# Optimization experiments

Hardware: AMD Instinct MI355X
Metric: run time of the kernel (lower is better)

The kernel has to match this reference:

```python
import jax, jax.numpy as jnp
import numpy as np

B, N, E, D, M, T, P, HS, HN, C, NH = 64, 1024, 512, 1024, 16, 12, 2048, 2048, 64, 4, 8
EPS = 1e-8


def _ln(x, g, b):
    m = x.mean(-1, keepdims=True)
    v = ((x - m) ** 2).mean(-1, keepdims=True)
    return (x - m) / jnp.sqrt(v + 1e-5) * g + b


def _glu(x):
    a, b = jnp.split(x, 2, axis=-1)
    return a * jax.nn.sigmoid(b)


def setup_inputs() -> dict:
    key = jax.random.key(0)
    ks = jax.random.split(key, 24)
    s = 0.02
    rn = lambda k, sh: jax.random.normal(k, sh, jnp.float32) * s
    inp = {
        'kv_tokens': jax.random.normal(ks[0], (B, N, E), jnp.float32),
        'raw_r_act': jnp.full((P,), -10.0, jnp.float32),  # no_decay_init
        'raw_r_out': jnp.full((P,), -10.0, jnp.float32),
        'q_w': rn(ks[1], (E, P)), 'q_b': jnp.zeros((E,), jnp.float32),
        'in_proj_w': rn(ks[2], (3 * E, E)), 'in_proj_b': jnp.zeros((3 * E,), jnp.float32),
        'out_proj_w': rn(ks[3], (E, E)), 'out_proj_b': jnp.zeros((E,), jnp.float32),
        'z_ln_g': jnp.ones((D,), jnp.float32), 'z_ln_b': jnp.zeros((D,), jnp.float32),
        'o_ln_g': jnp.ones((E,), jnp.float32), 'o_ln_b': jnp.zeros((E,), jnp.float32),
        'gate_w': rn(ks[4], (D, D + E)), 'gate_b': jnp.zeros((D,), jnp.float32),
        'cand_w': rn(ks[5], (D, D + E)), 'cand_b': jnp.zeros((D,), jnp.float32),
        'syn1_w': rn(ks[6], (HS, D + E)), 'syn1_b': jnp.zeros((HS,), jnp.float32),
        'syn2_w': rn(ks[7], (D, HS)), 'syn2_b': jnp.zeros((D,), jnp.float32),
        'nlm1_w': rn(ks[8], (D, M, 2 * HN)), 'nlm1_b': jnp.zeros((D, 2 * HN), jnp.float32),
        'nlm2_w': rn(ks[9], (D, HN, 2)), 'nlm2_b': jnp.zeros((D, 2), jnp.float32),
        'head_w': rn(ks[10], (C, P)), 'head_b': jnp.zeros((C,), jnp.float32),
        'act_left': jax.random.randint(ks[11], (P,), 0, D),
        'act_right': jax.random.randint(ks[12], (P,), 0, D),
        'out_left': jax.random.randint(ks[13], (P,), 0, D),
        'out_right': jax.random.randint(ks[14], (P,), 0, D),
    }
    return inp


def reference(kv_tokens, raw_r_act, raw_r_out, q_w, q_b, in_proj_w, in_proj_b,
              out_proj_w, out_proj_b, z_ln_g, z_ln_b, o_ln_g, o_ln_b,
              gate_w, gate_b, cand_w, cand_b, syn1_w, syn1_b, syn2_w, syn2_b,
              nlm1_w, nlm1_b, nlm2_w, nlm2_b, head_w, head_b,
              act_left, act_right, out_left, out_right):
    dh = E // NH
    scale = 1.0 / np.sqrt(dh).astype(np.float32)
    Wq, Wk, Wv = jnp.split(in_proj_w, 3, axis=0)
    bq, bk, bv = jnp.split(in_proj_b, 3, axis=0)
    # K/V are tick-invariant: project once.
    k = (kv_tokens @ Wk.T + bk).reshape(B, N, NH, dh).transpose(0, 2, 1, 3)  # [B,H,N,dh]
    v = (kv_tokens @ Wv.T + bv).reshape(B, N, NH, dh).transpose(0, 2, 1, 3)
    decay_a = jnp.exp(-jax.nn.softplus(raw_r_act))[None, :]
    decay_o = jnp.exp(-jax.nn.softplus(raw_r_out))[None, :]

    z0 = jnp.zeros((B, D), kv_tokens.dtype)
    A0 = jnp.zeros((B, D, M), kv_tokens.dtype)
    # init_state with z0 == 0 -> alpha 0, beta 1, synch 0
    a_a0 = z0[:, act_left] * z0[:, act_right]
    b_a0 = jnp.ones_like(a_a0)
    s_a0 = a_a0 / jnp.sqrt(b_a0 + EPS)
    a_o0 = z0[:, out_left] * z0[:, out_right]
    b_o0 = jnp.ones_like(a_o0)

    def tick(carry, _):
        z, A, a_a, b_a, s_a, a_o, b_o = carry
        # attention query from action sync
        q = s_a @ q_w.T + q_b                                  # [B,E]
        qh = (q @ Wq.T + bq).reshape(B, NH, 1, dh)
        scores = jnp.einsum('bhqd,bhnd->bhqn', qh, k) * scale  # [B,H,1,N]
        attn = jax.nn.softmax(scores, axis=-1)
        o = jnp.einsum('bhqn,bhnd->bhqd', attn, v).reshape(B, E)
        o = o @ out_proj_w.T + out_proj_b
        o = _ln(o, o_ln_g, o_ln_b)                             # LN on o
        zn = _ln(z, z_ln_g, z_ln_b)                            # LN on z
        # gated fusion
        u = jnp.concatenate([zn, o], axis=-1)
        g = jax.nn.sigmoid(u @ gate_w.T + gate_b)
        h = jnp.tanh(u @ cand_w.T + cand_b)
        z_bar = (1.0 - g) * zn + g * h
        fused = jnp.concatenate([z_bar, o], axis=-1)           # [B,D+E]
        # synapse MLP -> pre-activation
        pre = jax.nn.gelu(fused @ syn1_w.T + syn1_b, approximate=False) @ syn2_w.T + syn2_b
        A = jnp.concatenate([A[:, :, 1:], pre[:, :, None]], axis=-1)  # shift history
        # deep NLM (per-neuron SuperLinear + GLU, twice)
        h1 = _glu(jnp.einsum('bdm,dmh->bdh', A, nlm1_w) + nlm1_b)
        z = _glu(jnp.einsum('bdh,dho->bdo', h1, nlm2_w) + nlm2_b)[..., 0]
        # decayed pair synchronisation updates
        a_a = decay_a * a_a + z[:, act_left] * z[:, act_right]
        b_a = decay_a * b_a + 1.0
        s_a = a_a / jnp.sqrt(b_a + EPS)
        a_o = decay_o * a_o + z[:, out_left] * z[:, out_right]
        b_o = decay_o * b_o + 1.0
        s_o = a_o / jnp.sqrt(b_o + EPS)
        logits = s_o @ head_w.T + head_b                       # [B,C]
        return (z, A, a_a, b_a, s_a, a_o, b_o), (logits, z)

    carry0 = (z0, A0, a_a0, b_a0, s_a0, a_o0, b_o0)
    _, (logits_t, z_t) = jax.lax.scan(tick, carry0, None, length=T)
    logits_ticks = jnp.transpose(logits_t, (1, 2, 0))          # [B,C,T]
    p = jnp.clip(jax.nn.softmax(logits_ticks, axis=1), 1e-8, None)
    ent = -(p * jnp.log(p)).sum(axis=1)
    certainty = 1.0 - ent / np.float32(np.log(C))              # [B,T]
    z_ticks = jnp.transpose(z_t, (1, 0, 2))                    # [B,T,D]
    return logits_ticks, certainty, z_ticks
```

## Files before the change

kernel.cpp:

```cpp
#include <hip/hip_runtime.h>
#include <hip/hip_bf16.h>

#define B_ 64
#define N_ 1024
#define E_ 512
#define D_ 1024
#define M_ 16
#define T_ 12
#define P_ 2048
#define HS_ 2048
#define HN_ 64
#define C_ 4
#define NH_ 8
#define DH_ 64

typedef __attribute__((ext_vector_type(8))) short bf16x8;
typedef __attribute__((ext_vector_type(4))) float f32x4;

__device__ __forceinline__ float bf2f(unsigned int u) {
    union { unsigned int i; float f; } c; c.i = (u & 0xffffu) << 16; return c.f;
}
__device__ __forceinline__ unsigned short f2bf(float f) {
    union { float f; unsigned int i; } c; c.f = f;
    unsigned int x = c.i;
    unsigned int r = x + 0x7fffu + ((x >> 16) & 1u);
    return (unsigned short)(r >> 16);
}

__global__ void init_kernel(unsigned short* s_a_bf, float* a_a, float* b_a, float* a_o, float* b_o, float* z) {
    int i = blockIdx.x * 256 + threadIdx.x;
    if (i < B_ * P_) { a_a[i] = 0.f; b_a[i] = 1.f; a_o[i] = 0.f; b_o[i] = 1.f; s_a_bf[i] = 0; }
    if (i < B_ * D_) z[i] = 0.f;
}

__global__ __launch_bounds__(256) void cvt_bf16_kernel(const float* __restrict__ in,
                                                       unsigned short* __restrict__ out, int n4) {
    int i = blockIdx.x * 256 + threadIdx.x;
    if (i < n4) {
        float4 v = ((const float4*)in)[i];
        ushort4 o;
        o.x = f2bf(v.x); o.y = f2bf(v.y); o.z = f2bf(v.z); o.w = f2bf(v.w);
        ((ushort4*)out)[i] = o;
    }
}

__global__ __launch_bounds__(256) void cvt_ilv_kernel(const float* __restrict__ g,
                                                      const float* __restrict__ c,
                                                      unsigned short* __restrict__ out) {
    int r = blockIdx.x;
    const float* src = (r & 1) ? (c + (size_t)(r >> 1) * 1536) : (g + (size_t)(r >> 1) * 1536);
    for (int k = threadIdx.x * 4; k < 1536; k += 1024) {
        float4 v = *(const float4*)(src + k);
        ushort4 o;
        o.x = f2bf(v.x); o.y = f2bf(v.y); o.z = f2bf(v.z); o.w = f2bf(v.w);
        *(ushort4*)(out + (size_t)r * 1536 + k) = o;
    }
}

__global__ __launch_bounds__(256) void transpose_cvt_kernel(const float* __restrict__ in,
                                                            unsigned short* __restrict__ out,
                                                            int R, int Ccols) {
    __shared__ float tb[32][33];
    int c0 = blockIdx.x * 32, r0 = blockIdx.y * 32;
    int tx = threadIdx.x & 31, ty = threadIdx.x >> 5;
#pragma unroll
    for (int i = 0; i < 32; i += 8) tb[ty + i][tx] = in[(size_t)(r0 + ty + i) * Ccols + c0 + tx];
    __syncthreads();
#pragma unroll
    for (int i = 0; i < 32; i += 8) out[(size_t)(c0 + ty + i) * R + r0 + tx] = f2bf(tb[tx][ty + i]);
}

__global__ __launch_bounds__(256) void bcomb_kernel(const float* __restrict__ in_proj_w,
                                                    const float* __restrict__ in_proj_b,
                                                    const float* __restrict__ q_b,
                                                    float* __restrict__ bc) {
    int e = blockIdx.x * 256 + threadIdx.x;
    if (e < E_) {
        const float* wr = in_proj_w + (size_t)e * E_;
        float s = in_proj_b[e];
        for (int k = 0; k < E_; k += 4) {
            float4 w4 = *(const float4*)(wr + k);
            float4 q4 = *(const float4*)(q_b + k);
            s += w4.x * q4.x + w4.y * q4.y + w4.z * q4.z + w4.w * q4.w;
        }
        bc[e] = s;
    }
}

template <bool HAS_BIAS>
__global__ __launch_bounds__(256) void gemm_bt_kernel(const unsigned short* __restrict__ A,
                                                      const unsigned short* __restrict__ Bt,
                                                      const float* __restrict__ bias,
                                                      unsigned short* __restrict__ C,
                                                      int M, int N, int K) {
    __shared__ __align__(16) unsigned short ldsA[2][4096];
    __shared__ __align__(16) unsigned short ldsB[2][4096];
    int id = blockIdx.y * gridDim.x + blockIdx.x;
    int nwg = gridDim.x * gridDim.y;
    int swz = (id & 7) * (nwg >> 3) + (id >> 3);
    int bx = swz % gridDim.x, by = swz / gridDim.x;
    int m0 = by * 128;
    int n0 = bx * 128;
    int tid = threadIdx.x;
    int wv = tid >> 6, l = tid & 63;
    int wr = wv >> 1, wc = wv & 1;
    int lr = l & 15, lg = l >> 4;
    f32x4 acc[4][4] = {};

    auto stage = [&](int buf, int kt) {
        int k0 = kt * 32;
#pragma unroll
        for (int i = 0; i < 2; i++) {
            int tsk = tid + 256 * i;
            int r = tsk >> 2, g = tsk & 3;
            int gs = (g ^ (r & 3)) * 8;
            __builtin_amdgcn_global_load_lds(
                (const __attribute__((address_space(1))) void*)(A + (size_t)(m0 + r) * K + k0 + gs),
                (__attribute__((address_space(3))) void*)&ldsA[buf][tsk * 8], 16, 0, 0);
        }
#pragma unroll
        for (int i = 0; i < 2; i++) {
            int tsk = tid + 256 * i;
            int r = tsk >> 2, g = tsk & 3;
            int gs = (g ^ (r & 3)) * 8;
            __builtin_amdgcn_global_load_lds(
                (const __attribute__((address_space(1))) void*)(Bt + (size_t)(n0 + r) * K + k0 + gs),
                (__attribute__((address_space(3))) void*)&ldsB[buf][tsk * 8], 16, 0, 0);
        }
    };

    int nt = K >> 5;
    stage(0, 0);
    for (int t = 0; t < nt; t++) {
        int cur = t & 1;
        if (t + 1 < nt) {
            stage(cur ^ 1, t + 1);
            asm volatile("s_waitcnt vmcnt(4)" ::: "memory");
        } else {
            asm volatile("s_waitcnt vmcnt(0)" ::: "memory");
        }
        __builtin_amdgcn_s_barrier();
        bf16x8 af[4], bfr[4];
#pragma unroll
        for (int mi = 0; mi < 4; mi++) {
            int r = wr * 64 + mi * 16 + lr;
            af[mi] = *(const bf16x8*)&ldsA[cur][r * 32 + ((lg ^ (r & 3)) << 3)];
        }
#pragma unroll
        for (int ni = 0; ni < 4; ni++) {
            int c = wc * 64 + ni * 16 + lr;
            bfr[ni] = *(const bf16x8*)&ldsB[cur][c * 32 + ((lg ^ (c & 3)) << 3)];
        }
#pragma unroll
        for (int mi = 0; mi < 4; mi++)
#pragma unroll
            for (int ni = 0; ni < 4; ni++)
                acc[mi][ni] = __builtin_amdgcn_mfma_f32_16x16x32_bf16(af[mi], bfr[ni], acc[mi][ni], 0, 0, 0);
        __builtin_amdgcn_s_barrier();
    }
#pragma unroll
    for (int ni = 0; ni < 4; ni++) {
        int col = n0 + wc * 64 + ni * 16 + lr;
        float bv = HAS_BIAS ? bias[col] : 0.0f;
#pragma unroll
        for (int mi = 0; mi < 4; mi++) {
            int row = m0 + wr * 64 + mi * 16 + lg * 4;
#pragma unroll
            for (int r = 0; r < 4; r++) {
                C[(size_t)(row + r) * N + col] = f2bf(acc[mi][ni][r] + bv);
            }
        }
    }
}

template <int EPI>
__global__ __launch_bounds__(256) void gemmNK_kernel(const unsigned short* __restrict__ A,
                                                     const unsigned short* __restrict__ W,
                                                     const float* __restrict__ bias0,
                                                     const float* __restrict__ bias1,
                                                     const float* __restrict__ zn32,
                                                     void* __restrict__ outp,
                                                     int N, int K) {
    __shared__ __align__(16) unsigned short ldsA[4][2][2048];
    __shared__ __align__(16) unsigned short ldsB[4][2][512];
    int n0 = blockIdx.x * 16;
    int tid = threadIdx.x;
    int w = tid >> 6, l = tid & 63;
    int Kw = K >> 2;
    int kb = w * Kw;
    int lr = l & 15, lg = l >> 4;
    int ar = l >> 2, ag = l & 3;
    f32x4 acc[4] = {};

    auto stage = [&](int buf, int kt) {
        int k0 = kb + (kt << 5);
#pragma unroll
        for (int i = 0; i < 4; i++) {
            int row = i * 16 + ar;
            int gs = (ag ^ (row & 3)) << 3;
            __builtin_amdgcn_global_load_lds(
                (const __attribute__((address_space(1))) void*)(A + (size_t)row * K + k0 + gs),
                (__attribute__((address_space(3))) void*)&ldsA[w][buf][i * 512 + l * 8], 16, 0, 0);
        }
        {
            int col = ar;
            int gs = (ag ^ (col & 3)) << 3;
            __builtin_amdgcn_global_load_lds(
                (const __attribute__((address_space(1))) void*)(W + (size_t)(n0 + col) * K + k0 + gs),
                (__attribute__((address_space(3))) void*)&ldsB[w][buf][l * 8], 16, 0, 0);
        }
    };

    int nt = Kw >> 5;
    stage(0, 0);
    for (int t = 0; t < nt; t++) {
        int cur = t & 1;
        if (t + 1 < nt) {
            stage(cur ^ 1, t + 1);
            asm volatile("s_waitcnt vmcnt(5)" ::: "memory");
        } else {
            asm volatile("s_waitcnt vmcnt(0)" ::: "memory");
        }
        bf16x8 bf = *(const bf16x8*)&ldsB[w][cur][lr * 32 + ((lg ^ (lr & 3)) << 3)];
#pragma unroll
        for (int mi = 0; mi < 4; mi++) {
            int rr = mi * 16 + lr;
            bf16x8 af = *(const bf16x8*)&ldsA[w][cur][rr * 32 + ((lg ^ (rr & 3)) << 3)];
            acc[mi] = __builtin_amdgcn_mfma_f32_16x16x32_bf16(af, bf, acc[mi], 0, 0, 0);
        }
    }
    __syncthreads();
    float* red = (float*)&ldsA[0][0][0];
#pragma unroll
    for (int mi = 0; mi < 4; mi++) {
        int row = mi * 16 + lg * 4;
#pragma unroll
        for (int q = 0; q < 4; q++) red[w * 1024 + (row + q) * 16 + lr] = acc[mi][q];
    }
    __syncthreads();
    int b = tid >> 2, c4 = (tid & 3) << 2;
    f32x4 s = *(f32x4*)&red[b * 16 + c4];
#pragma unroll
    for (int ww = 1; ww < 4; ww++) {
        f32x4 v = *(f32x4*)&red[ww * 1024 + b * 16 + c4];
        s[0] += v[0]; s[1] += v[1]; s[2] += v[2]; s[3] += v[3];
    }
    int col = n0 + c4;
    if (EPI == 0) {
        unsigned short* out = (unsigned short*)outp;
        ushort4 o;
        o.x = f2bf(s[0] + bias0[col + 0]);
        o.y = f2bf(s[1] + bias0[col + 1]);
        o.z = f2bf(s[2] + bias0[col + 2]);
        o.w = f2bf(s[3] + bias0[col + 3]);
        *(ushort4*)(out + (size_t)b * N + col) = o;
    } else if (EPI == 1) {
        float* out = (float*)outp;
        *(f32x4*)(out + (size_t)b * N + col) = s;
    } else if (EPI == 2) {
        unsigned short* out = (unsigned short*)outp;
        int j0 = col >> 1;
#pragma unroll
        for (int pp = 0; pp < 2; pp++) {
            int j = j0 + pp;
            float g = 1.0f / (1.0f + expf(-(s[pp * 2] + bias0[j])));
            float h = tanhf(s[pp * 2 + 1] + bias1[j]);
            float zb = (1.0f - g) * zn32[(size_t)b * D_ + j] + g * h;
            out[(size_t)b * 1536 + j] = f2bf(zb);
        }
    } else if (EPI == 3) {
        unsigned short* out = (unsigned short*)outp;
        ushort4 o;
#pragma unroll
        for (int j = 0; j < 4; j++) {
            float pre = s[j] + bias0[col + j];
            float val = 0.5f * pre * (1.0f + erff(pre * 0.70710678118654752f));
            ((unsigned short*)&o)[j] = f2bf(val);
        }
        *(ushort4*)(out + (size_t)b * N + col) = o;
    } else {
        float* out = (float*)outp;
#pragma unroll
        for (int j = 0; j < 4; j++) {
            out[(size_t)(col + j) * 64 + b] = s[j] + bias0[col + j];
        }
    }
}

__device__ __forceinline__ float wave_max64(float v) {
#pragma unroll
    for (int off = 32; off >= 1; off >>= 1) v = fmaxf(v, __shfl_xor(v, off, 64));
    return v;
}
__device__ __forceinline__ float wave_sum64(float v) {
#pragma unroll
    for (int off = 32; off >= 1; off >>= 1) v += __shfl_xor(v, off, 64);
    return v;
}

__global__ __launch_bounds__(256) void attn_kernel(const unsigned short* __restrict__ kvbuf,
                                                   const unsigned short* __restrict__ qh_bf,
                                                   unsigned short* __restrict__ o_bf) {
    int bh = blockIdx.x;
    int b = bh >> 3, h = bh & 7;
    __shared__ float sc[N_];
    __shared__ float qv[DH_];
    __shared__ float red[8];
    __shared__ float opart[4][DH_];
    int tid = threadIdx.x;
    int w = tid >> 6, lane = tid & 63;
    if (tid < DH_) qv[tid] = bf2f(qh_bf[(size_t)b * E_ + h * DH_ + tid]);
    __syncthreads();
    const unsigned short* kb = kvbuf + (size_t)b * N_ * 1024 + h * DH_;
    float myv[4];
#pragma unroll
    for (int i = 0; i < 4; i++) {
        int n = tid + i * 256;
        const unsigned short* kr = kb + (size_t)n * 1024;
        float s = 0.f;
#pragma unroll
        for (int d = 0; d < DH_; d += 8) {
            uint4 pk = *(const uint4*)(kr + d);
            s += bf2f(pk.x) * qv[d + 0] + bf2f(pk.x >> 16) * qv[d + 1]
               + bf2f(pk.y) * qv[d + 2] + bf2f(pk.y >> 16) * qv[d + 3]
               + bf2f(pk.z) * qv[d + 4] + bf2f(pk.z >> 16) * qv[d + 5]
               + bf2f(pk.w) * qv[d + 6] + bf2f(pk.w >> 16) * qv[d + 7];
        }
        myv[i] = s * 0.125f;
    }
    float m = fmaxf(fmaxf(myv[0], myv[1]), fmaxf(myv[2], myv[3]));
    m = wave_max64(m);
    if (lane == 0) red[w] = m;
    __syncthreads();
    m = fmaxf(fmaxf(red[0], red[1]), fmaxf(red[2], red[3]));
    float s = 0.f;
#pragma unroll
    for (int i = 0; i < 4; i++) {
        float e = expf(myv[i] - m);
        sc[tid + i * 256] = e;
        s += e;
    }
    s = wave_sum64(s);
    if (lane == 0) red[4 + w] = s;
    __syncthreads();
    float inv = 1.0f / (red[4] + red[5] + red[6] + red[7]);
    const unsigned short* vb = kvbuf + (size_t)b * N_ * 1024 + E_ + h * DH_;
    int ng = lane >> 4, d4 = (lane & 15) << 2;
    float a0 = 0.f, a1 = 0.f, a2 = 0.f, a3 = 0.f;
    int n0 = w * 256;
    for (int i = 0; i < 64; i++) {
        int n = n0 + i * 4 + ng;
        uint2 pv = *(const uint2*)(vb + (size_t)n * 1024 + d4);
        float sv = sc[n];
        a0 += sv * bf2f(pv.x);
        a1 += sv * bf2f(pv.x >> 16);
        a2 += sv * bf2f(pv.y);
        a3 += sv * bf2f(pv.y >> 16);
    }
    a0 += __shfl_xor(a0, 16, 64); a0 += __shfl_xor(a0, 32, 64);
    a1 += __shfl_xor(a1, 16, 64); a1 += __shfl_xor(a1, 32, 64);
    a2 += __shfl_xor(a2, 16, 64); a2 += __shfl_xor(a2, 32, 64);
    a3 += __shfl_xor(a3, 16, 64); a3 += __shfl_xor(a3, 32, 64);
    if (lane < 16) {
        opart[w][d4 + 0] = a0;
        opart[w][d4 + 1] = a1;
        opart[w][d4 + 2] = a2;
        opart[w][d4 + 3] = a3;
    }
    __syncthreads();
    if (tid < DH_) {
        float r = (opart[0][tid] + opart[1][tid] + opart[2][tid] + opart[3][tid]) * inv;
        o_bf[(size_t)b * E_ + h * DH_ + tid] = f2bf(r);
    }
}

__global__ __launch_bounds__(256) void reduce_oln_kernel(const float* __restrict__ opre,
                                                         const float* __restrict__ bout,
                                                         const float* __restrict__ og,
                                                         const float* __restrict__ obv,
                                                         const float* __restrict__ z,
                                                         const float* __restrict__ zg,
                                                         const float* __restrict__ zbv,
                                                         unsigned short* __restrict__ u_bf,
                                                         unsigned short* __restrict__ fused_bf,
                                                         float* __restrict__ zn32) {
    int b = blockIdx.x, tid = threadIdx.x;
    __shared__ float red[16];
    float v[2];
#pragma unroll
    for (int i = 0; i < 2; i++) {
        int e = tid + i * 256;
        v[i] = opre[(size_t)b * E_ + e] + bout[e];
    }
    int w = tid >> 6, lane = tid & 63;
    float s1 = v[0] + v[1];
    float s2 = v[0] * v[0] + v[1] * v[1];
#pragma unroll
    for (int off = 32; off >= 1; off >>= 1) { s1 += __shfl_xor(s1, off, 64); s2 += __shfl_xor(s2, off, 64); }
    if (lane == 0) { red[w] = s1; red[4 + w] = s2; }
    __syncthreads();
    s1 = red[0] + red[1] + red[2] + red[3];
    s2 = red[4] + red[5] + red[6] + red[7];
    float mean = s1 * (1.0f / 512.0f);
    float var = s2 * (1.0f / 512.0f) - mean * mean;
    float rstd = 1.0f / sqrtf(var + 1e-5f);
#pragma unroll
    for (int i = 0; i < 2; i++) {
        int e = tid + i * 256;
        unsigned short val = f2bf((v[i] - mean) * rstd * og[e] + obv[e]);
        u_bf[(size_t)b * 1536 + D_ + e] = val;
        fused_bf[(size_t)b * 1536 + D_ + e] = val;
    }
    float zl[4];
    float t1 = 0.f, t2 = 0.f;
#pragma unroll
    for (int i = 0; i < 4; i++) {
        int d = tid + i * 256;
        zl[i] = z[(size_t)b * D_ + d];
        t1 += zl[i]; t2 += zl[i] * zl[i];
    }
#pragma unroll
    for (int off = 32; off >= 1; off >>= 1) { t1 += __shfl_xor(t1, off, 64); t2 += __shfl_xor(t2, off, 64); }
    __syncthreads();
    if (lane == 0) { red[8 + w] = t1; red[12 + w] = t2; }
    __syncthreads();
    t1 = red[8] + red[9] + red[10] + red[11];
    t2 = red[12] + red[13] + red[14] + red[15];
    float zmean = t1 * (1.0f / 1024.0f);
    float zvar = t2 * (1.0f / 1024.0f) - zmean * zmean;
    float zr = 1.0f / sqrtf(zvar + 1e-5f);
#pragma unroll
    for (int i = 0; i < 4; i++) {
        int d = tid + i * 256;
        float zn = (zl[i] - zmean) * zr * zg[d] + zbv[d];
        u_bf[(size_t)b * 1536 + d] = f2bf(zn);
        zn32[(size_t)b * D_ + d] = zn;
    }
}

template <int NT>
__global__ __launch_bounds__(256) void nlm_kernel(const float* __restrict__ AbufT,
                                                  const float* __restrict__ w1g,
                                                  const float* __restrict__ b1g,
                                                  const float* __restrict__ w2g,
                                                  const float* __restrict__ b2g,
                                                  float* __restrict__ z,
                                                  float* __restrict__ zt) {
    __shared__ float w1s[4][2048];
    __shared__ float b1s[4][128];
    __shared__ float w2s[4][128];
    __shared__ float b2s[4][2];
    int tid = threadIdx.x;
    int w = tid >> 6, lane = tid & 63;
    int d = blockIdx.x * 4 + w;
    for (int i = lane; i < 2048; i += 64) w1s[w][i] = w1g[(size_t)d * 2048 + i];
    for (int i = lane; i < 128; i += 64) {
        b1s[w][i] = b1g[(size_t)d * 128 + i];
        w2s[w][i] = w2g[(size_t)d * 128 + i];
    }
    if (lane < 2) b2s[w][lane] = b2g[d * 2 + lane];
    __syncthreads();
    const int b = lane;
    float av[NT];
#pragma unroll
    for (int s = 0; s < NT; s++) av[s] = AbufT[((size_t)s * D_ + d) * 64 + b];
    constexpr int moff = M_ - NT;
    float o0 = b2s[w][0], o1 = b2s[w][1];
    for (int hh = 0; hh < 64; hh++) {
        float a = b1s[w][hh], bb = b1s[w][hh + 64];
#pragma unroll
        for (int s = 0; s < NT; s++) {
            float x = av[s];
            a += x * w1s[w][(s + moff) * 128 + hh];
            bb += x * w1s[w][(s + moff) * 128 + hh + 64];
        }
        float z1 = a / (1.0f + expf(-bb));
        o0 += z1 * w2s[w][hh * 2];
        o1 += z1 * w2s[w][hh * 2 + 1];
    }
    float zv = o0 / (1.0f + expf(-o1));
    z[(size_t)b * D_ + d] = zv;
    zt[((size_t)b * T_ + (NT - 1)) * D_ + d] = zv;
}

__global__ __launch_bounds__(256) void synchead_kernel(const float* __restrict__ z,
                                                       const int* __restrict__ act_l, const int* __restrict__ act_r,
                                                       const int* __restrict__ out_l, const int* __restrict__ out_r,
                                                       const float* __restrict__ raw_a, const float* __restrict__ raw_o,
                                                       const float* __restrict__ head_w, const float* __restrict__ head_b,
                                                       float* __restrict__ a_a, float* __restrict__ b_a,
                                                       unsigned short* __restrict__ s_a_bf,
                                                       float* __restrict__ a_o, float* __restrict__ b_o,
                                                       float* __restrict__ out_logits, float* __restrict__ out_cert, int t) {
    int b = blockIdx.x, tid = threadIdx.x;
    __shared__ float zv[D_];
    __shared__ float red[4][4];
    for (int i = tid; i < D_; i += 256) zv[i] = z[(size_t)b * D_ + i];
    __syncthreads();
    float l0 = 0.f, l1 = 0.f, l2 = 0.f, l3 = 0.f;
    for (int p = tid; p < P_; p += 256) {
        size_t ip = (size_t)b * P_ + p;
        float zl = zv[act_l[p]], zr = zv[act_r[p]];
        float da = 1.0f / (1.0f + expf(raw_a[p]));
        float aa = da * a_a[ip] + zl * zr;
        float ba = da * b_a[ip] + 1.0f;
        a_a[ip] = aa; b_a[ip] = ba;
        s_a_bf[(size_t)b * P_ + p] = f2bf(aa / sqrtf(ba + 1e-8f));
        float zlo = zv[out_l[p]], zro = zv[out_r[p]];
        float dz = 1.0f / (1.0f + expf(raw_o[p]));
        float ao = dz * a_o[ip] + zlo * zro;
        float bo = dz * b_o[ip] + 1.0f;
        a_o[ip] = ao; b_o[ip] = bo;
        float so = ao / sqrtf(bo + 1e-8f);
        l0 += so * head_w[p];
        l1 += so * head_w[P_ + p];
        l2 += so * head_w[2 * P_ + p];
        l3 += so * head_w[3 * P_ + p];
    }
    int w = tid >> 6, lane = tid & 63;
#pragma unroll
    for (int off = 32; off >= 1; off >>= 1) {
        l0 += __shfl_xor(l0, off, 64);
        l1 += __shfl_xor(l1, off, 64);
        l2 += __shfl_xor(l2, off, 64);
        l3 += __shfl_xor(l3, off, 64);
    }
    if (lane == 0) { red[w][0] = l0; red[w][1] = l1; red[w][2] = l2; red[w][3] = l3; }
    __syncthreads();
    if (tid == 0) {
        float lg[4];
#pragma unroll
        for (int c = 0; c < 4; c++) {
            lg[c] = red[0][c] + red[1][c] + red[2][c] + red[3][c] + head_b[c];
            out_logits[((size_t)b * C_ + c) * T_ + t] = lg[c];
        }
        float m = fmaxf(fmaxf(lg[0], lg[1]), fmaxf(lg[2], lg[3]));
        float e0 = expf(lg[0] - m), e1 = expf(lg[1] - m), e2 = expf(lg[2] - m), e3 = expf(lg[3] - m);
        float inv = 1.0f / (e0 + e1 + e2 + e3);
        float ent = 0.f, pp;
        pp = fmaxf(e0 * inv, 1e-8f); ent -= pp * logf(pp);
        pp = fmaxf(e1 * inv, 1e-8f); ent -= pp * logf(pp);
        pp = fmaxf(e2 * inv, 1e-8f); ent -= pp * logf(pp);
        pp = fmaxf(e3 * inv, 1e-8f); ent -= pp * logf(pp);
        out_cert[(size_t)b * T_ + t] = 1.0f - ent * (1.0f / 1.3862943611198906f);
    }
}

extern "C" void kernel_launch(void* const* d_in, const int* in_sizes, int n_in,
                              void* d_out, int out_size, void* d_ws, size_t ws_size,
                              hipStream_t stream) {
    const float* kv_tokens  = (const float*)d_in[0];
    const float* raw_r_act  = (const float*)d_in[1];
    const float* raw_r_out  = (const float*)d_in[2];
    const float* q_w        = (const float*)d_in[3];
    const float* q_b        = (const float*)d_in[4];
    const float* in_proj_w  = (const float*)d_in[5];
    const float* in_proj_b  = (const float*)d_in[6];
    const float* out_proj_w = (const float*)d_in[7];
    const float* out_proj_b = (const float*)d_in[8];
    const float* z_ln_g     = (const float*)d_in[9];
    const float* z_ln_b     = (const float*)d_in[10];
    const float* o_ln_g     = (const float*)d_in[11];
    const float* o_ln_b     = (const float*)d_in[12];
    const float* gate_w     = (const float*)d_in[13];
    const float* gate_b     = (const float*)d_in[14];
    const float* cand_w     = (const float*)d_in[15];
    const float* cand_b     = (const float*)d_in[16];
    const float* syn1_w     = (const float*)d_in[17];
    const float* syn1_b     = (const float*)d_in[18];
    const float* syn2_w     = (const float*)d_in[19];
    const float* syn2_b     = (const float*)d_in[20];
    const float* nlm1_w     = (const float*)d_in[21];
    const float* nlm1_b     = (const float*)d_in[22];
    const float* nlm2_w     = (const float*)d_in[23];
    const float* nlm2_b     = (const float*)d_in[24];
    const float* head_w     = (const float*)d_in[25];
    const float* head_b     = (const float*)d_in[26];
    const int* act_l        = (const int*)d_in[27];
    const int* act_r        = (const int*)d_in[28];
    const int* out_l        = (const int*)d_in[29];
    const int* out_r        = (const int*)d_in[30];

    float* out = (float*)d_out;
    float* out_logits = out;
    float* out_cert = out + B_ * C_ * T_;
    float* out_zt = out_cert + B_ * T_;

    char* ws = (char*)d_ws;
    size_t off = 0;
    auto alloc = [&](size_t bytes) { void* p = ws + off; off += (bytes + 255) & ~(size_t)255; return p; };
    unsigned short* kvbuf   = (unsigned short*)alloc((size_t)B_ * N_ * 1024 * 2);
    unsigned short* kv_bf   = (unsigned short*)alloc((size_t)B_ * N_ * E_ * 2);
    unsigned short* Wkv_bf  = (unsigned short*)alloc((size_t)1024 * E_ * 2);
    unsigned short* Wq_bf   = (unsigned short*)alloc((size_t)E_ * E_ * 2);
    unsigned short* qwT_bf  = (unsigned short*)alloc((size_t)P_ * E_ * 2);
    unsigned short* Wc_bf   = (unsigned short*)alloc((size_t)E_ * P_ * 2);
    unsigned short* Wgc_bf  = (unsigned short*)alloc((size_t)2048 * 1536 * 2);
    unsigned short* Ws1_bf  = (unsigned short*)alloc((size_t)2048 * 1536 * 2);
    unsigned short* Ws2_bf  = (unsigned short*)alloc((size_t)1024 * 2048 * 2);
    unsigned short* Wout_bf = (unsigned short*)alloc((size_t)E_ * E_ * 2);
    float* b_comb = (float*)alloc(E_ * 4);
    unsigned short* s_a_bf  = (unsigned short*)alloc((size_t)B_ * P_ * 2);
    unsigned short* qh_bf   = (unsigned short*)alloc((size_t)B_ * E_ * 2);
    unsigned short* o_bf    = (unsigned short*)alloc((size_t)B_ * E_ * 2);
    unsigned short* u_bf    = (unsigned short*)alloc((size_t)B_ * 1536 * 2);
    unsigned short* fused_bf= (unsigned short*)alloc((size_t)B_ * 1536 * 2);
    unsigned short* tbuf_bf = (unsigned short*)alloc((size_t)B_ * HS_ * 2);
    float* opre = (float*)alloc((size_t)B_ * E_ * 4);
    float* zn32 = (float*)alloc((size_t)B_ * D_ * 4);
    float* a_a  = (float*)alloc((size_t)B_ * P_ * 4);
    float* b_a  = (float*)alloc((size_t)B_ * P_ * 4);
    float* a_o  = (float*)alloc((size_t)B_ * P_ * 4);
    float* b_o  = (float*)alloc((size_t)B_ * P_ * 4);
    float* zbuf = (float*)alloc((size_t)B_ * D_ * 4);
    float* AbufT = (float*)alloc((size_t)T_ * D_ * B_ * 4);

    init_kernel<<<512, 256, 0, stream>>>(s_a_bf, a_a, b_a, a_o, b_o, zbuf);

    cvt_bf16_kernel<<<(1024 * E_ / 4 + 255) / 256, 256, 0, stream>>>(in_proj_w + (size_t)E_ * E_, Wkv_bf, 1024 * E_ / 4);
    cvt_bf16_kernel<<<(E_ * E_ / 4 + 255) / 256, 256, 0, stream>>>(in_proj_w, Wq_bf, E_ * E_ / 4);
    cvt_ilv_kernel<<<2048, 256, 0, stream>>>(gate_w, cand_w, Wgc_bf);
    cvt_bf16_kernel<<<(2048 * 1536 / 4 + 255) / 256, 256, 0, stream>>>(syn1_w, Ws1_bf, 2048 * 1536 / 4);
    cvt_bf16_kernel<<<(1024 * 2048 / 4 + 255) / 256, 256, 0, stream>>>(syn2_w, Ws2_bf, 1024 * 2048 / 4);
    cvt_bf16_kernel<<<(E_ * E_ / 4 + 255) / 256, 256, 0, stream>>>(out_proj_w, Wout_bf, E_ * E_ / 4);
    transpose_cvt_kernel<<<dim3(P_ / 32, E_ / 32), 256, 0, stream>>>(q_w, qwT_bf, E_, P_);
    bcomb_kernel<<<2, 256, 0, stream>>>(in_proj_w, in_proj_b, q_b, b_comb);
    gemm_bt_kernel<false><<<dim3(P_ / 128, E_ / 128), 256, 0, stream>>>(Wq_bf, qwT_bf, nullptr, Wc_bf, E_, P_, E_);

    cvt_bf16_kernel<<<(B_ * N_ * E_ / 4) / 256, 256, 0, stream>>>(kv_tokens, kv_bf, B_ * N_ * E_ / 4);
    gemm_bt_kernel<true><<<dim3(8, 512), 256, 0, stream>>>(kv_bf, Wkv_bf, in_proj_b + E_,
                                                           kvbuf, B_ * N_, 1024, E_);

    for (int t = 0; t < T_; t++) {
        gemmNK_kernel<0><<<32, 256, 0, stream>>>(s_a_bf, Wc_bf, b_comb, nullptr, nullptr, qh_bf, E_, P_);
        attn_kernel<<<B_ * NH_, 256, 0, stream>>>(kvbuf, qh_bf, o_bf);
        gemmNK_kernel<1><<<32, 256, 0, stream>>>(o_bf, Wout_bf, nullptr, nullptr, nullptr, opre, E_, E_);
        reduce_oln_kernel<<<64, 256, 0, stream>>>(opre, out_proj_b, o_ln_g, o_ln_b,
                                                  zbuf, z_ln_g, z_ln_b, u_bf, fused_bf, zn32);
        gemmNK_kernel<2><<<128, 256, 0, stream>>>(u_bf, Wgc_bf, gate_b, cand_b, zn32, fused_bf, 2048, 1536);
        gemmNK_kernel<3><<<128, 256, 0, stream>>>(fused_bf, Ws1_bf, syn1_b, nullptr, nullptr, tbuf_bf, 2048, 1536);
        gemmNK_kernel<4><<<64, 256, 0, stream>>>(tbuf_bf, Ws2_bf, syn2_b, nullptr, nullptr,
                                                 AbufT + (size_t)t * D_ * 64, 1024, 2048);
        switch (t) {
            case 0:  nlm_kernel<1><<<256, 256, 0, stream>>>(AbufT, nlm1_w, nlm1_b, nlm2_w, nlm2_b, zbuf, out_zt); break;
            case 1:  nlm_kernel<2><<<256, 256, 0, stream>>>(AbufT, nlm1_w, nlm1_b, nlm2_w, nlm2_b, zbuf, out_zt); break;
            case 2:  nlm_kernel<3><<<256, 256, 0, stream>>>(AbufT, nlm1_w, nlm1_b, nlm2_w, nlm2_b, zbuf, out_zt); break;
            case 3:  nlm_kernel<4><<<256, 256, 0, stream>>>(AbufT, nlm1_w, nlm1_b, nlm2_w, nlm2_b, zbuf, out_zt); break;
            case 4:  nlm_kernel<5><<<256, 256, 0, stream>>>(AbufT, nlm1_w, nlm1_b, nlm2_w, nlm2_b, zbuf, out_zt); break;
            case 5:  nlm_kernel<6><<<256, 256, 0, stream>>>(AbufT, nlm1_w, nlm1_b, nlm2_w, nlm2_b, zbuf, out_zt); break;
            case 6:  nlm_kernel<7><<<256, 256, 0, stream>>>(AbufT, nlm1_w, nlm1_b, nlm2_w, nlm2_b, zbuf, out_zt); break;
            case 7:  nlm_kernel<8><<<256, 256, 0, stream>>>(AbufT, nlm1_w, nlm1_b, nlm2_w, nlm2_b, zbuf, out_zt); break;
            case 8:  nlm_kernel<9><<<256, 256, 0, stream>>>(AbufT, nlm1_w, nlm1_b, nlm2_w, nlm2_b, zbuf, out_zt); break;
            case 9:  nlm_kernel<10><<<256, 256, 0, stream>>>(AbufT, nlm1_w, nlm1_b, nlm2_w, nlm2_b, zbuf, out_zt); break;
            case 10: nlm_kernel<11><<<256, 256, 0, stream>>>(AbufT, nlm1_w, nlm1_b, nlm2_w, nlm2_b, zbuf, out_zt); break;
            default: nlm_kernel<12><<<256, 256, 0, stream>>>(AbufT, nlm1_w, nlm1_b, nlm2_w, nlm2_b, zbuf, out_zt); break;
        }
        synchead_kernel<<<64, 256, 0, stream>>>(zbuf, act_l, act_r, out_l, out_r, raw_r_act, raw_r_out,
                                                head_w, head_b, a_a, b_a, s_a_bf, a_o, b_o,
                                                out_logits, out_cert, t);
    }
}
```

Measured before the change: 1.438 ms.

## Fuse query projection into attention, out-proj into LN, bf16 NLM weights, deeper swizzle

Result: slower. 1.749 ms (+21.6%).

```diff
diff --git a/kernel.cpp b/kernel.cpp
--- a/kernel.cpp
+++ b/kernel.cpp
@@ -25,6 +25,12 @@
     unsigned int x = c.i;
     unsigned int r = x + 0x7fffu + ((x >> 16) & 1u);
     return (unsigned short)(r >> 16);
+}
+__device__ __forceinline__ float dot2bf(unsigned int a, unsigned int b) {
+    union { unsigned int i; float f; } al, ah, bl, bh;
+    al.i = a << 16; ah.i = a & 0xffff0000u;
+    bl.i = b << 16; bh.i = b & 0xffff0000u;
+    return al.f * bl.f + ah.f * bh.f;
 }
 
 __global__ void init_kernel(unsigned short* s_a_bf, float* a_a, float* b_a, float* a_o, float* b_o, float* z) {
@@ -113,7 +119,7 @@
         for (int i = 0; i < 2; i++) {
             int tsk = tid + 256 * i;
             int r = tsk >> 2, g = tsk & 3;
-            int gs = (g ^ (r & 3)) * 8;
+            int gs = (g ^ (r & 3) ^ ((r >> 2) & 3)) * 8;
             __builtin_amdgcn_global_load_lds(
                 (const __attribute__((address_space(1))) void*)(A + (size_t)(m0 + r) * K + k0 + gs),
                 (__attribute__((address_space(3))) void*)&ldsA[buf][tsk * 8], 16, 0, 0);
@@ -122,7 +128,7 @@
         for (int i = 0; i < 2; i++) {
             int tsk = tid + 256 * i;
             int r = tsk >> 2, g = tsk & 3;
-            int gs = (g ^ (r & 3)) * 8;
+            int gs = (g ^ (r & 3) ^ ((r >> 2) & 3)) * 8;
             __builtin_amdgcn_global_load_lds(
                 (const __attribute__((address_space(1))) void*)(Bt + (size_t)(n0 + r) * K + k0 + gs),
                 (__attribute__((address_space(3))) void*)&ldsB[buf][tsk * 8], 16, 0, 0);
@@ -144,12 +150,14 @@
 #pragma unroll
         for (int mi = 0; mi < 4; mi++) {
             int r = wr * 64 + mi * 16 + lr;
-            af[mi] = *(const bf16x8*)&ldsA[cur][r * 32 + ((lg ^ (r & 3)) << 3)];
+            int slot = lg ^ (r & 3) ^ ((r >> 2) & 3);
+            af[mi] = *(const bf16x8*)&ldsA[cur][r * 32 + (slot << 3)];
         }
 #pragma unroll
         for (int ni = 0; ni < 4; ni++) {
             int c = wc * 64 + ni * 16 + lr;
-            bfr[ni] = *(const bf16x8*)&ldsB[cur][c * 32 + ((lg ^ (c & 3)) << 3)];
+            int slot = lg ^ (c & 3) ^ ((c >> 2) & 3);
+            bfr[ni] = *(const bf16x8*)&ldsB[cur][c * 32 + (slot << 3)];
         }
 #pragma unroll
         for (int mi = 0; mi < 4; mi++)
@@ -197,14 +205,14 @@
 #pragma unroll
         for (int i = 0; i < 4; i++) {
             int row = i * 16 + ar;
-            int gs = (ag ^ (row & 3)) << 3;
+            int gs = (ag ^ (row & 3) ^ ((row >> 2) & 3)) << 3;
             __builtin_amdgcn_global_load_lds(
                 (const __attribute__((address_space(1))) void*)(A + (size_t)row * K + k0 + gs),
                 (__attribute__((address_space(3))) void*)&ldsA[w][buf][i * 512 + l * 8], 16, 0, 0);
         }
         {
             int col = ar;
-            int gs = (ag ^ (col & 3)) << 3;
+            int gs = (ag ^ (col & 3) ^ ((col >> 2) & 3)) << 3;
             __builtin_amdgcn_global_load_lds(
                 (const __attribute__((address_space(1))) void*)(W + (size_t)(n0 + col) * K + k0 + gs),
                 (__attribute__((address_space(3))) void*)&ldsB[w][buf][l * 8], 16, 0, 0);
@@ -221,11 +229,13 @@
         } else {
             asm volatile("s_waitcnt vmcnt(0)" ::: "memory");
         }
-        bf16x8 bf = *(const bf16x8*)&ldsB[w][cur][lr * 32 + ((lg ^ (lr & 3)) << 3)];
+        int bslot = lg ^ (lr & 3) ^ ((lr >> 2) & 3);
+        bf16x8 bf = *(const bf16x8*)&ldsB[w][cur][lr * 32 + (bslot << 3)];
 #pragma unroll
         for (int mi = 0; mi < 4; mi++) {
             int rr = mi * 16 + lr;
-            bf16x8 af = *(const bf16x8*)&ldsA[w][cur][rr * 32 + ((lg ^ (rr & 3)) << 3)];
+            int slot = lg ^ (rr & 3) ^ ((rr >> 2) & 3);
+            bf16x8 af = *(const bf16x8*)&ldsA[w][cur][rr * 32 + (slot << 3)];
             acc[mi] = __builtin_amdgcn_mfma_f32_16x16x32_bf16(af, bf, acc[mi], 0, 0, 0);
         }
     }
@@ -246,18 +256,7 @@
         s[0] += v[0]; s[1] += v[1]; s[2] += v[2]; s[3] += v[3];
     }
     int col = n0 + c4;
-    if (EPI == 0) {
-        unsigned short* out = (unsigned short*)outp;
-        ushort4 o;
-        o.x = f2bf(s[0] + bias0[col + 0]);
-        o.y = f2bf(s[1] + bias0[col + 1]);
-        o.z = f2bf(s[2] + bias0[col + 2]);
-        o.w = f2bf(s[3] + bias0[col + 3]);
-        *(ushort4*)(out + (size_t)b * N + col) = o;
-    } else if (EPI == 1) {
-        float* out = (float*)outp;
-        *(f32x4*)(out + (size_t)b * N + col) = s;
-    } else if (EPI == 2) {
+    if (EPI == 2) {
         unsigned short* out = (unsigned short*)outp;
         int j0 = col >> 1;
 #pragma unroll
@@ -287,19 +286,10 @@
     }
 }
 
-__device__ __forceinline__ float wave_max64(float v) {
-#pragma unroll
-    for (int off = 32; off >= 1; off >>= 1) v = fmaxf(v, __shfl_xor(v, off, 64));
-    return v;
-}
-__device__ __forceinline__ float wave_sum64(float v) {
-#pragma unroll
-    for (int off = 32; off >= 1; off >>= 1) v += __shfl_xor(v, off, 64);
-    return v;
-}
-
 __global__ __launch_bounds__(256) void attn_kernel(const unsigned short* __restrict__ kvbuf,
-                                                   const unsigned short* __restrict__ qh_bf,
+                                                   const unsigned short* __restrict__ s_a_bf,
+                                                   const unsigned short* __restrict__ Wc_bf,
+                                                   const float* __restrict__ b_comb,
                                                    unsigned short* __restrict__ o_bf) {
     int bh = blockIdx.x;
     int b = bh >> 3, h = bh & 7;
@@ -309,7 +299,24 @@
     __shared__ float opart[4][DH_];
     int tid = threadIdx.x;
     int w = tid >> 6, lane = tid & 63;
-    if (tid < DH_) qv[tid] = bf2f(qh_bf[(size_t)b * E_ + h * DH_ + tid]);
+    uint4 sa[4];
+#pragma unroll
+    for (int i = 0; i < 4; i++)
+        sa[i] = *(const uint4*)(s_a_bf + (size_t)b * P_ + i * 512 + lane * 8);
+    for (int cg = 0; cg < 16; cg++) {
+        int col = cg * 4 + w;
+        const unsigned short* wr = Wc_bf + (size_t)(h * 64 + col) * P_;
+        float acc = 0.f;
+#pragma unroll
+        for (int i = 0; i < 4; i++) {
+            uint4 wv = *(const uint4*)(wr + i * 512 + lane * 8);
+            acc += dot2bf(wv.x, sa[i].x) + dot2bf(wv.y, sa[i].y)
+                 + dot2bf(wv.z, sa[i].z) + dot2bf(wv.w, sa[i].w);
+        }
+#pragma unroll
+        for (int off = 32; off >= 1; off >>= 1) acc += __shfl_xor(acc, off, 64);
+        if (lane == 0) qv[col] = acc + b_comb[h * 64 + col];
+    }
     __syncthreads();
     const unsigned short* kb = kvbuf + (size_t)b * N_ * 1024 + h * DH_;
     float myv[4];
@@ -329,7 +336,8 @@
         myv[i] = s * 0.125f;
     }
     float m = fmaxf(fmaxf(myv[0], myv[1]), fmaxf(myv[2], myv[3]));
-    m = wave_max64(m);
+#pragma unroll
+    for (int off = 32; off >= 1; off >>= 1) m = fmaxf(m, __shfl_xor(m, off, 64));
     if (lane == 0) red[w] = m;
     __syncthreads();
     m = fmaxf(fmaxf(red[0], red[1]), fmaxf(red[2], red[3]));
@@ -340,17 +348,18 @@
         sc[tid + i * 256] = e;
         s += e;
     }
-    s = wave_sum64(s);
+#pragma unroll
+    for (int off = 32; off >= 1; off >>= 1) s += __shfl_xor(s, off, 64);
     if (lane == 0) red[4 + w] = s;
     __syncthreads();
     float inv = 1.0f / (red[4] + red[5] + red[6] + red[7]);
-    const unsigned short* vb = kvbuf + (size_t)b * N_ * 1024 + E_ + h * DH_;
+    const unsigned short* vbp = kvbuf + (size_t)b * N_ * 1024 + E_ + h * DH_;
     int ng = lane >> 4, d4 = (lane & 15) << 2;
     float a0 = 0.f, a1 = 0.f, a2 = 0.f, a3 = 0.f;
     int n0 = w * 256;
     for (int i = 0; i < 64; i++) {
         int n = n0 + i * 4 + ng;
-        uint2 pv = *(const uint2*)(vb + (size_t)n * 1024 + d4);
+        uint2 pv = *(const uint2*)(vbp + (size_t)n * 1024 + d4);
         float sv = sc[n];
         a0 += sv * bf2f(pv.x);
         a1 += sv * bf2f(pv.x >> 16);
@@ -374,27 +383,40 @@
     }
 }
 
-__global__ __launch_bounds__(256) void reduce_oln_kernel(const float* __restrict__ opre,
-                                                         const float* __restrict__ bout,
-                                                         const float* __restrict__ og,
-                                                         const float* __restrict__ obv,
-                                                         const float* __restrict__ z,
-                                                         const float* __restrict__ zg,
-                                                         const float* __restrict__ zbv,
-                                                         unsigned short* __restrict__ u_bf,
-                                                         unsigned short* __restrict__ fused_bf,
-                                                         float* __restrict__ zn32) {
+__global__ __launch_bounds__(256) void oproj_oln_kernel(const unsigned short* __restrict__ o_bf,
+                                                        const unsigned short* __restrict__ WoutT_bf,
+                                                        const float* __restrict__ bout,
+                                                        const float* __restrict__ og,
+                                                        const float* __restrict__ obv,
+                                                        const float* __restrict__ z,
+                                                        const float* __restrict__ zg,
+                                                        const float* __restrict__ zbv,
+                                                        unsigned short* __restrict__ u_bf,
+                                                        unsigned short* __restrict__ fused_bf,
+                                                        float* __restrict__ zn32) {
     int b = blockIdx.x, tid = threadIdx.x;
+    __shared__ float ov[E_];
     __shared__ float red[16];
-    float v[2];
-#pragma unroll
-    for (int i = 0; i < 2; i++) {
-        int e = tid + i * 256;
-        v[i] = opre[(size_t)b * E_ + e] + bout[e];
-    }
+    {
+        unsigned int pk = *(const unsigned int*)(o_bf + (size_t)b * E_ + tid * 2);
+        ov[tid * 2] = bf2f(pk);
+        ov[tid * 2 + 1] = bf2f(pk >> 16);
+    }
+    __syncthreads();
+    int e0 = tid * 2;
+    float v0 = 0.f, v1 = 0.f;
+#pragma unroll 8
+    for (int k = 0; k < E_; k++) {
+        unsigned int pk = *(const unsigned int*)(WoutT_bf + (size_t)k * E_ + e0);
+        float o = ov[k];
+        v0 += o * bf2f(pk);
+        v1 += o * bf2f(pk >> 16);
+    }
+    v0 += bout[e0];
+    v1 += bout[e0 + 1];
     int w = tid >> 6, lane = tid & 63;
-    float s1 = v[0] + v[1];
-    float s2 = v[0] * v[0] + v[1] * v[1];
+    float s1 = v0 + v1;
+    float s2 = v0 * v0 + v1 * v1;
 #pragma unroll
     for (int off = 32; off >= 1; off >>= 1) { s1 += __shfl_xor(s1, off, 64); s2 += __shfl_xor(s2, off, 64); }
     if (lane == 0) { red[w] = s1; red[4 + w] = s2; }
@@ -404,12 +426,11 @@
     float mean = s1 * (1.0f / 512.0f);
     float var = s2 * (1.0f / 512.0f) - mean * mean;
     float rstd = 1.0f / sqrtf(var + 1e-5f);
-#pragma unroll
-    for (int i = 0; i < 2; i++) {
-        int e = tid + i * 256;
-        unsigned short val = f2bf((v[i] - mean) * rstd * og[e] + obv[e]);
-        u_bf[(size_t)b * 1536 + D_ + e] = val;
-        fused_bf[(size_t)b * 1536 + D_ + e] = val;
+    {
+        unsigned int pk = (unsigned int)f2bf((v0 - mean) * rstd * og[e0] + obv[e0])
+                        | ((unsigned int)f2bf((v1 - mean) * rstd * og[e0 + 1] + obv[e0 + 1]) << 16);
+        *(unsigned int*)(u_bf + (size_t)b * 1536 + D_ + e0) = pk;
+        *(unsigned int*)(fused_bf + (size_t)b * 1536 + D_ + e0) = pk;
     }
     float zl[4];
     float t1 = 0.f, t2 = 0.f;
@@ -440,7 +461,7 @@
 
 template <int NT>
 __global__ __launch_bounds__(256) void nlm_kernel(const float* __restrict__ AbufT,
-                                                  const float* __restrict__ w1g,
+                                                  const unsigned short* __restrict__ w1g_bf,
                                                   const float* __restrict__ b1g,
                                                   const float* __restrict__ w2g,
                                                   const float* __restrict__ b2g,
@@ -453,7 +474,11 @@
     int tid = threadIdx.x;
     int w = tid >> 6, lane = tid & 63;
     int d = blockIdx.x * 4 + w;
-    for (int i = lane; i < 2048; i += 64) w1s[w][i] = w1g[(size_t)d * 2048 + i];
+    for (int i = lane * 2; i < 2048; i += 128) {
+        unsigned int pk = *(const unsigned int*)(w1g_bf + (size_t)d * 2048 + i);
+        w1s[w][i] = bf2f(pk);
+        w1s[w][i + 1] = bf2f(pk >> 16);
+    }
     for (int i = lane; i < 128; i += 64) {
         b1s[w][i] = b1g[(size_t)d * 128 + i];
         w2s[w][i] = w2g[(size_t)d * 128 + i];
@@ -598,15 +623,14 @@
     unsigned short* Wgc_bf  = (unsigned short*)alloc((size_t)2048 * 1536 * 2);
     unsigned short* Ws1_bf  = (unsigned short*)alloc((size_t)2048 * 1536 * 2);
     unsigned short* Ws2_bf  = (unsigned short*)alloc((size_t)1024 * 2048 * 2);
-    unsigned short* Wout_bf = (unsigned short*)alloc((size_t)E_ * E_ * 2);
+    unsigned short* WoutT_bf= (unsigned short*)alloc((size_t)E_ * E_ * 2);
+    unsigned short* nlm1w_bf= (unsigned short*)alloc((size_t)1024 * 2048 * 2);
     float* b_comb = (float*)alloc(E_ * 4);
     unsigned short* s_a_bf  = (unsigned short*)alloc((size_t)B_ * P_ * 2);
-    unsigned short* qh_bf   = (unsigned short*)alloc((size_t)B_ * E_ * 2);
     unsigned short* o_bf    = (unsigned short*)alloc((size_t)B_ * E_ * 2);
     unsigned short* u_bf    = (unsigned short*)alloc((size_t)B_ * 1536 * 2);
     unsigned short* fused_bf= (unsigned short*)alloc((size_t)B_ * 1536 * 2);
     unsigned short* tbuf_bf = (unsigned short*)alloc((size_t)B_ * HS_ * 2);
-    float* opre = (float*)alloc((size_t)B_ * E_ * 4);
     float* zn32 = (float*)alloc((size_t)B_ * D_ * 4);
     float* a_a  = (float*)alloc((size_t)B_ * P_ * 4);
     float* b_a  = (float*)alloc((size_t)B_ * P_ * 4);
@@ -622,7 +646,8 @@
     cvt_ilv_kernel<<<2048, 256, 0, stream>>>(gate_w, cand_w, Wgc_bf);
     cvt_bf16_kernel<<<(2048 * 1536 / 4 + 255) / 256, 256, 0, stream>>>(syn1_w, Ws1_bf, 2048 * 1536 / 4);
     cvt_bf16_kernel<<<(1024 * 2048 / 4 + 255) / 256, 256, 0, stream>>>(syn2_w, Ws2_bf, 1024 * 2048 / 4);
-    cvt_bf16_kernel<<<(E_ * E_ / 4 + 255) / 256, 256, 0, stream>>>(out_proj_w, Wout_bf, E_ * E_ / 4);
+    cvt_bf16_kernel<<<(1024 * 2048 / 4 + 255) / 256, 256, 0, stream>>>(nlm1_w, nlm1w_bf, 1024 * 2048 / 4);
+    transpose_cvt_kernel<<<dim3(E_ / 32, E_ / 32), 256, 0, stream>>>(out_proj_w, WoutT_bf, E_, E_);
     transpose_cvt_kernel<<<dim3(P_ / 32, E_ / 32), 256, 0, stream>>>(q_w, qwT_bf, E_, P_);
     bcomb_kernel<<<2, 256, 0, stream>>>(in_proj_w, in_proj_b, q_b, b_comb);
     gemm_bt_kernel<false><<<dim3(P_ / 128, E_ / 128), 256, 0, stream>>>(Wq_bf, qwT_bf, nullptr, Wc_bf, E_, P_, E_);
@@ -632,28 +657,26 @@
                                                            kvbuf, B_ * N_, 1024, E_);
 
     for (int t = 0; t < T_; t++) {
-        gemmNK_kernel<0><<<32, 256, 0, stream>>>(s_a_bf, Wc_bf, b_comb, nullptr, nullptr, qh_bf, E_, P_);
-        attn_kernel<<<B_ * NH_, 256, 0, stream>>>(kvbuf, qh_bf, o_bf);
-        gemmNK_kernel<1><<<32, 256, 0, stream>>>(o_bf, Wout_bf, nullptr, nullptr, nullptr, opre, E_, E_);
-        reduce_oln_kernel<<<64, 256, 0, stream>>>(opre, out_proj_b, o_ln_g, o_ln_b,
-                                                  zbuf, z_ln_g, z_ln_b, u_bf, fused_bf, zn32);
+        attn_kernel<<<B_ * NH_, 256, 0, stream>>>(kvbuf, s_a_bf, Wc_bf, b_comb, o_bf);
+        oproj_oln_kernel<<<64, 256, 0, stream>>>(o_bf, WoutT_bf, out_proj_b, o_ln_g, o_ln_b,
+                                                 zbuf, z_ln_g, z_ln_b, u_bf, fused_bf, zn32);
         gemmNK_kernel<2><<<128, 256, 0, stream>>>(u_bf, Wgc_bf, gate_b, cand_b, zn32, fused_bf, 2048, 1536);
         gemmNK_kernel<3><<<128, 256, 0, stream>>>(fused_bf, Ws1_bf, syn1_b, nullptr, nullptr, tbuf_bf, 2048, 1536);
         gemmNK_kernel<4><<<64, 256, 0, stream>>>(tbuf_bf, Ws2_bf, syn2_b, nullptr, nullptr,
                                                  AbufT + (size_t)t * D_ * 64, 1024, 2048);
         switch (t) {
-            case 0:  nlm_kernel<1><<<256, 256, 0, stream>>>(AbufT, nlm1_w, nlm1_b, nlm2_w, nlm2_b, zbuf, out_zt); break;
-            case 1:  nlm_kernel<2><<<256, 256, 0, stream>>>(AbufT, nlm1_w, nlm1_b, nlm2_w, nlm2_b, zbuf, out_zt); break;
-            case 2:  nlm_kernel<3><<<256, 256, 0, stream>>>(AbufT, nlm1_w, nlm1_b, nlm2_w, nlm2_b, zbuf, out_zt); break;
-            case 3:  nlm_kernel<4><<<256, 256, 0, stream>>>(AbufT, nlm1_w, nlm1_b, nlm2_w, nlm2_b, zbuf, out_zt); break;
-            case 4:  nlm_kernel<5><<<256, 256, 0, stream>>>(AbufT, nlm1_w, nlm1_b, nlm2_w, nlm2_b, zbuf, out_zt); break;
-            case 5:  nlm_kernel<6><<<256, 256, 0, stream>>>(AbufT, nlm1_w, nlm1_b, nlm2_w, nlm2_b, zbuf, out_zt); break;
-            case 6:  nlm_kernel<7><<<256, 256, 0, stream>>>(AbufT, nlm1_w, nlm1_b, nlm2_w, nlm2_b, zbuf, out_zt); break;
-            case 7:  nlm_kernel<8><<<256, 256, 0, stream>>>(AbufT, nlm1_w, nlm1_b, nlm2_w, nlm2_b, zbuf, out_zt); break;
-            case 8:  nlm_kernel<9><<<256, 256, 0, stream>>>(AbufT, nlm1_w, nlm1_b, nlm2_w, nlm2_b, zbuf, out_zt); break;
-            case 9:  nlm_kernel<10><<<256, 256, 0, stream>>>(AbufT, nlm1_w, nlm1_b, nlm2_w, nlm2_b, zbuf, out_zt); break;
-            case 10: nlm_kernel<11><<<256, 256, 0, stream>>>(AbufT, nlm1_w, nlm1_b, nlm2_w, nlm2_b, zbuf, out_zt); break;
-            default: nlm_kernel<12><<<256, 256, 0, stream>>>(AbufT, nlm1_w, nlm1_b, nlm2_w, nlm2_b, zbuf, out_zt); break;
+            case 0:  nlm_kernel<1><<<256, 256, 0, stream>>>(AbufT, nlm1w_bf, nlm1_b, nlm2_w, nlm2_b, zbuf, out_zt); break;
+            case 1:  nlm_kernel<2><<<256, 256, 0, stream>>>(AbufT, nlm1w_bf, nlm1_b, nlm2_w, nlm2_b, zbuf, out_zt); break;
+            case 2:  nlm_kernel<3><<<256, 256, 0, stream>>>(AbufT, nlm1w_bf, nlm1_b, nlm2_w, nlm2_b, zbuf, out_zt); break;
+            case 3:  nlm_kernel<4><<<256, 256, 0, stream>>>(AbufT, nlm1w_bf, nlm1_b, nlm2_w, nlm2_b, zbuf, out_zt); break;
+            case 4:  nlm_kernel<5><<<256, 256, 0, stream>>>(AbufT, nlm1w_bf, nlm1_b, nlm2_w, nlm2_b, zbuf, out_zt); break;
+            case 5:  nlm_kernel<6><<<256, 256, 0, stream>>>(AbufT, nlm1w_bf, nlm1_b, nlm2_w, nlm2_b, zbuf, out_zt); break;
+            case 6:  nlm_kernel<7><<<256, 256, 0, stream>>>(AbufT, nlm1w_bf, nlm1_b, nlm2_w, nlm2_b, zbuf, out_zt); break;
+            case 7:  nlm_kernel<8><<<256, 256, 0, stream>>>(AbufT, nlm1w_bf, nlm1_b, nlm2_w, nlm2_b, zbuf, out_zt); break;
+            case 8:  nlm_kernel<9><<<256, 256, 0, stream>>>(AbufT, nlm1w_bf, nlm1_b, nlm2_w, nlm2_b, zbuf, out_zt); break;
+            case 9:  nlm_kernel<10><<<256, 256, 0, stream>>>(AbufT, nlm1w_bf, nlm1_b, nlm2_w, nlm2_b, zbuf, out_zt); break;
+            case 10: nlm_kernel<11><<<256, 256, 0, stream>>>(AbufT, nlm1w_bf, nlm1_b, nlm2_w, nlm2_b, zbuf, out_zt); break;
+            default: nlm_kernel<12><<<256, 256, 0, stream>>>(AbufT, nlm1w_bf, nlm1_b, nlm2_w, nlm2_b, zbuf, out_zt); break;
         }
         synchead_kernel<<<64, 256, 0, stream>>>(zbuf, act_l, act_r, out_l, out_r, raw_r_act, raw_r_out,
                                                 head_w, head_b, a_a, b_a, s_a_bf, a_o, b_o,
```
